# Kernel tuning notes

Measured on AMD Instinct MI355X. Metric: run time of the kernel, lower is better.

The kernel has to match this reference:

```python
import jax, jax.numpy as jnp
import numpy as np
from jax.ops import segment_sum, segment_max

DIM = 64
NUM_FEAT = 14
EDGE_FEAT = 4
OUT_DIM = 16
NUM_GRAPHS = 512
NEG_SLOPE = 0.01


def _leaky(v):
    return jnp.where(v >= 0, v, NEG_SLOPE * v)


def setup_inputs() -> dict:
    key = jax.random.key(0)
    ks = jax.random.split(key, 24)
    N, E = 20000, 40000
    s = 0.1
    inp = {
        "x": jax.random.normal(ks[0], (N, NUM_FEAT), jnp.float32),
        "edge_attr": jax.random.normal(ks[1], (E, EDGE_FEAT), jnp.float32),
        "edge_index": jax.random.randint(ks[2], (2, E), 0, N, jnp.int64) if jax.config.jax_enable_x64 else jax.random.randint(ks[2], (2, E), 0, N).astype(jnp.int32),
        "batch": jnp.sort(jax.random.randint(ks[3], (N,), 0, NUM_GRAPHS)).astype(jnp.int32),
        # lin0
        "lin0_w": s * jax.random.normal(ks[4], (DIM, NUM_FEAT), jnp.float32),
        "lin0_b": s * jax.random.normal(ks[5], (DIM,), jnp.float32),
        # edge network: Linear(4,dim) -> LeakyReLU -> Linear(dim, dim*dim)
        "net_w1": s * jax.random.normal(ks[6], (DIM, EDGE_FEAT), jnp.float32),
        "net_b1": s * jax.random.normal(ks[7], (DIM,), jnp.float32),
        "net_w2": s * jax.random.normal(ks[8], (DIM * DIM, DIM), jnp.float32),
        "net_b2": s * jax.random.normal(ks[9], (DIM * DIM,), jnp.float32),
        # NNConv root weight + bias
        "root_w": s * jax.random.normal(ks[10], (DIM, DIM), jnp.float32),
        "conv_b": s * jax.random.normal(ks[11], (DIM,), jnp.float32),
        # GRU (torch gate order: r, z, n)
        "gru_w_ih": s * jax.random.normal(ks[12], (3 * DIM, DIM), jnp.float32),
        "gru_w_hh": s * jax.random.normal(ks[13], (3 * DIM, DIM), jnp.float32),
        "gru_b_ih": s * jax.random.normal(ks[14], (3 * DIM,), jnp.float32),
        "gru_b_hh": s * jax.random.normal(ks[15], (3 * DIM,), jnp.float32),
        # Set2Set LSTM (input 2*dim, hidden dim; torch gate order: i, f, g, o)
        "lstm_w_ih": s * jax.random.normal(ks[16], (4 * DIM, 2 * DIM), jnp.float32),
        "lstm_w_hh": s * jax.random.normal(ks[17], (4 * DIM, DIM), jnp.float32),
        "lstm_b_ih": s * jax.random.normal(ks[18], (4 * DIM,), jnp.float32),
        "lstm_b_hh": s * jax.random.normal(ks[19], (4 * DIM,), jnp.float32),
        # lin_out
        "lout_w": s * jax.random.normal(ks[20], (OUT_DIM, 2 * DIM), jnp.float32),
        "lout_b": s * jax.random.normal(ks[21], (OUT_DIM,), jnp.float32),
    }
    return inp


def _forward(x, edge_attr, lin0_w, lin0_b, net_w1, net_b1, net_w2, net_b2,
             root_w, conv_b, gru_w_ih, gru_w_hh, gru_b_ih, gru_b_hh,
             lstm_w_ih, lstm_w_hh, lstm_b_ih, lstm_b_hh, lout_w, lout_b,
             edge_index, batch):
    N = x.shape[0]
    src, tgt = edge_index[0], edge_index[1]

    # per-edge dim x dim weight (shared across the 6 steps; edge_attr is static)
    ew = _leaky(edge_attr @ net_w1.T + net_b1) @ net_w2.T + net_b2  # [E, dim*dim]
    ew = ew.reshape(-1, DIM, DIM)  # [E, in, out]

    deg = segment_sum(jnp.ones_like(tgt, jnp.float32), tgt, num_segments=N)
    inv_deg = 1.0 / jnp.maximum(deg, 1.0)

    out = _leaky(x @ lin0_w.T + lin0_b)  # [N, dim]
    h = out
    for _ in range(6):
        msg = jnp.einsum('ed,edo->eo', out[src], ew)  # gather + per-edge matvec
        agg = segment_sum(msg, tgt, num_segments=N) * inv_deg[:, None]  # scatter-mean
        conv = agg + out @ root_w + conv_b
        m = _leaky(conv)
        # GRU cell (seq len 1)
        gi = m @ gru_w_ih.T + gru_b_ih
        gh = h @ gru_w_hh.T + gru_b_hh
        gi_r, gi_z, gi_n = jnp.split(gi, 3, axis=-1)
        gh_r, gh_z, gh_n = jnp.split(gh, 3, axis=-1)
        r = jax.nn.sigmoid(gi_r + gh_r)
        z = jax.nn.sigmoid(gi_z + gh_z)
        n = jnp.tanh(gi_n + r * gh_n)
        h = (1.0 - z) * n + z * h
        out = h

    # Set2Set, processing_steps=1
    B = NUM_GRAPHS
    q_star = jnp.zeros((B, 2 * DIM), x.dtype)
    h_l = jnp.zeros((B, DIM), x.dtype)
    c_l = jnp.zeros((B, DIM), x.dtype)
    gates = q_star @ lstm_w_ih.T + lstm_b_ih + h_l @ lstm_w_hh.T + lstm_b_hh
    gi_, gf_, gg_, go_ = jnp.split(gates, 4, axis=-1)
    i_g = jax.nn.sigmoid(gi_)
    f_g = jax.nn.sigmoid(gf_)
    g_g = jnp.tanh(gg_)
    o_g = jax.nn.sigmoid(go_)
    c = f_g * c_l + i_g * g_g
    q = o_g * jnp.tanh(c)  # [B, dim]

    e = jnp.sum(out * q[batch], axis=-1)  # [N]
    emax = segment_max(e, batch, num_segments=B)
    emax = jnp.where(jnp.isfinite(emax), emax, 0.0)
    ex = jnp.exp(e - emax[batch])
    denom = segment_sum(ex, batch, num_segments=B)
    a = ex / jnp.maximum(denom, 1e-16)[batch]
    r_read = segment_sum(a[:, None] * out, batch, num_segments=B)  # [B, dim]
    q_star = jnp.concatenate([q, r_read], axis=-1)  # [B, 2*dim]

    return q_star @ lout_w.T + lout_b  # [B, out_dim]


def reference(x, edge_attr, edge_index, batch, lin0_w, lin0_b, net_w1, net_b1,
              net_w2, net_b2, root_w, conv_b, gru_w_ih, gru_w_hh, gru_b_ih,
              gru_b_hh, lstm_w_ih, lstm_w_hh, lstm_b_ih, lstm_b_hh, lout_w, lout_b):
    return _forward(x, edge_attr, lin0_w, lin0_b, net_w1, net_b1, net_w2, net_b2,
                    root_w, conv_b, gru_w_ih, gru_w_hh, gru_b_ih, gru_b_hh,
                    lstm_w_ih, lstm_w_hh, lstm_b_ih, lstm_b_hh, lout_w, lout_b,
                    edge_index, batch)
```

## Files before the change

kernel.cpp:

```cpp
#include <hip/hip_runtime.h>
#include <math.h>

#define DIM 64
#define NFEAT 14
#define EFEAT 4
#define ODIM 16
#define NGRAPH 512
#define NEG 0.01f
#define EBLK 128
#define DSPLIT 4

typedef _Float16 f16;
typedef _Float16 f16x8 __attribute__((ext_vector_type(8)));
typedef float f32x4 __attribute__((ext_vector_type(4)));

#define MFMA(a,b,c) __builtin_amdgcn_mfma_f32_16x16x32_f16(a,b,c,0,0,0)

__device__ __forceinline__ float leaky(float v){ return v >= 0.f ? v : NEG*v; }
__device__ __forceinline__ float sigm(float v){ return 1.f/(1.f+expf(-v)); }

__global__ void k_pack(const float* __restrict__ src, f16* __restrict__ dst, int NC, int transB){
    int i = blockIdx.x*blockDim.x + threadIdx.x;
    if (i >= NC*64) return;
    int j = i & 7, l = (i >> 3) & 63, s = (i >> 9) & 1, CT = i >> 10;
    int k = ((l >> 4) << 3) + 32*s + j;
    int c = CT*16 + (l & 15);
    float v = transB ? src[(size_t)k*NC + c] : src[(size_t)c*64 + k];
    dst[i] = (f16)v;
}

__global__ void k_hid(const float* __restrict__ ea, const float* __restrict__ w1,
                      const float* __restrict__ b1, f16* __restrict__ hid16, int E){
    int i = blockIdx.x*blockDim.x + threadIdx.x;
    if (i >= E*DIM) return;
    int e = i >> 6, k = i & 63;
    const float* a = ea + (size_t)e*EFEAT;
    const float* w = w1 + k*EFEAT;
    float v = b1[k] + a[0]*w[0] + a[1]*w[1] + a[2]*w[2] + a[3]*w[3];
    hid16[i] = (f16)leaky(v);
}

__global__ void k_deg(const int* __restrict__ ei, float* __restrict__ deg, int E){
    int e = blockIdx.x*blockDim.x + threadIdx.x;
    if (e < E) atomicAdd(&deg[ei[E + e]], 1.0f);
}

__global__ void k_invdeg(float* __restrict__ deg, int N){
    int i = blockIdx.x*blockDim.x + threadIdx.x;
    if (i < N) deg[i] = 1.0f / fmaxf(deg[i], 1.0f);
}

__global__ void k_lin0(const float* __restrict__ x, const float* __restrict__ w,
                       const float* __restrict__ b, float* __restrict__ hf,
                       f16* __restrict__ out16, int N){
    int i = blockIdx.x*blockDim.x + threadIdx.x;
    if (i >= N*DIM) return;
    int n = i >> 6, o = i & 63;
    const float* xr = x + (size_t)n*NFEAT;
    const float* wr = w + o*NFEAT;
    float v = b[o];
#pragma unroll
    for (int f = 0; f < NFEAT; ++f) v += xr[f]*wr[f];
    v = leaky(v);
    hf[i] = v; out16[i] = (f16)v;
}

__global__ __launch_bounds__(256) void k_nbias(const f16x8* __restrict__ out16v,
                                               const f16x8* __restrict__ b2f,
                                               float* __restrict__ nb, int N){
    int n0 = blockIdx.x*64;
    int tid = threadIdx.x, w = tid >> 6, l = tid & 63, li = l & 15, lh = l >> 4;
    int ar = n0 + 16*w + li;
    f16x8 a0{}, a1{};
    if (ar < N){ a0 = out16v[(size_t)ar*8 + lh]; a1 = out16v[(size_t)ar*8 + lh + 4]; }
    f32x4 z = {0.f,0.f,0.f,0.f};
#pragma unroll
    for (int ct = 0; ct < 4; ++ct){
        f32x4 p = MFMA(a0, b2f[(ct*2+0)*64 + l], z);
        p = MFMA(a1, b2f[(ct*2+1)*64 + l], p);
#pragma unroll
        for (int reg = 0; reg < 4; ++reg){
            int n = n0 + 16*w + lh*4 + reg;
            if (n < N) nb[(size_t)n*64 + ct*16 + li] = p[reg];
        }
    }
}

__global__ __launch_bounds__(256) void k_fmsg(const float* __restrict__ hf,
                                              const f16x8* __restrict__ hid16v,
                                              const f16x8* __restrict__ wpf,
                                              const float* __restrict__ nb,
                                              const int* __restrict__ ei,
                                              float* __restrict__ agg, int E){
    __shared__ float Os[EBLK][20];
    __shared__ int ssrc[EBLK];
    __shared__ int stgt[EBLK];
    int tid = threadIdx.x;
    int e0 = blockIdx.x*EBLK;
    int dz = blockIdx.y;
    int d0 = dz*16;
    if (tid < EBLK){
        int e = e0 + tid;
        ssrc[tid] = (e < E) ? ei[e] : -1;
        stgt[tid] = (e < E) ? ei[E + e] : -1;
    }
    __syncthreads();
    for (int i = tid; i < EBLK*16; i += 256){
        int row = i >> 4, dl = i & 15;
        int s = ssrc[row];
        Os[row][dl] = (s >= 0) ? hf[(size_t)s*64 + d0 + dl] : 0.f;
    }

    int w = tid >> 6, l = tid & 63, li = l & 15, lh = l >> 4;
    f16x8 a[2][2];
#pragma unroll
    for (int rt = 0; rt < 2; ++rt){
        int e = e0 + w*32 + rt*16 + li;
        if (e < E){
            a[rt][0] = hid16v[(size_t)e*8 + lh];
            a[rt][1] = hid16v[(size_t)e*8 + lh + 4];
        } else { a[rt][0] = f16x8{}; a[rt][1] = f16x8{}; }
    }
    __syncthreads();

    float acc[2][4][4] = {};
    f32x4 z = {0.f,0.f,0.f,0.f};

#pragma unroll 2
    for (int dd = 0; dd < 16; ++dd){
        const f16x8* wrow = wpf + ((size_t)(d0 + dd))*512;
        f16x8 b[4][2];
#pragma unroll
        for (int ct = 0; ct < 4; ++ct){
            b[ct][0] = wrow[(ct*2+0)*64 + l];
            b[ct][1] = wrow[(ct*2+1)*64 + l];
        }
        float osv[2][4];
#pragma unroll
        for (int rt = 0; rt < 2; ++rt)
#pragma unroll
            for (int reg = 0; reg < 4; ++reg)
                osv[rt][reg] = Os[w*32 + rt*16 + lh*4 + reg][dd];
#pragma unroll
        for (int rt = 0; rt < 2; ++rt){
#pragma unroll
            for (int ct = 0; ct < 4; ++ct){
                f32x4 p = MFMA(a[rt][0], b[ct][0], z);
                p = MFMA(a[rt][1], b[ct][1], p);
#pragma unroll
                for (int reg = 0; reg < 4; ++reg)
                    acc[rt][ct][reg] += osv[rt][reg]*p[reg];
            }
        }
    }

#pragma unroll
    for (int rt = 0; rt < 2; ++rt){
#pragma unroll
        for (int reg = 0; reg < 4; ++reg){
            int row = w*32 + rt*16 + lh*4 + reg;
            int t = stgt[row];
            if (t < 0) continue;
            int s = ssrc[row];
#pragma unroll
            for (int ct = 0; ct < 4; ++ct){
                int col = ct*16 + li;
                float v = acc[rt][ct][reg];
                if (dz == 0) v += nb[(size_t)s*64 + col];
                atomicAdd(&agg[(size_t)t*64 + col], v);
            }
        }
    }
}

__global__ __launch_bounds__(256) void k_node(float* __restrict__ hf,
                                              f16* __restrict__ out16,
                                              const f16x8* __restrict__ out16v,
                                              float* __restrict__ agg,
                                              const float* __restrict__ invdeg,
                                              const float* __restrict__ convb,
                                              const f16x8* __restrict__ wrf,
                                              const f16x8* __restrict__ wihf,
                                              const f16x8* __restrict__ whhf,
                                              const float* __restrict__ bih,
                                              const float* __restrict__ bhh,
                                              const f16x8* __restrict__ b2f,
                                              float* __restrict__ nb, int N){
    __shared__ f16 Ms[64][72];
    int n0 = blockIdx.x*64;
    int tid = threadIdx.x, w = tid >> 6, l = tid & 63, li = l & 15, lh = l >> 4;
    f32x4 z = {0.f,0.f,0.f,0.f};

    int ar = n0 + 16*w + li;
    f16x8 a0{}, a1{};
    if (ar < N){ a0 = out16v[(size_t)ar*8 + lh]; a1 = out16v[(size_t)ar*8 + lh + 4]; }

    int nrow[4]; float invd[4];
#pragma unroll
    for (int reg = 0; reg < 4; ++reg){
        nrow[reg] = n0 + 16*w + lh*4 + reg;
        invd[reg] = (nrow[reg] < N) ? invdeg[nrow[reg]] : 0.f;
    }

#pragma unroll
    for (int ct = 0; ct < 4; ++ct){
        f32x4 p = MFMA(a0, wrf[(ct*2+0)*64 + l], z);
        p = MFMA(a1, wrf[(ct*2+1)*64 + l], p);
        int col = ct*16 + li;
        float cb = convb[col];
#pragma unroll
        for (int reg = 0; reg < 4; ++reg){
            int n = nrow[reg];
            float m = 0.f;
            if (n < N){
                size_t idx = (size_t)n*64 + col;
                m = leaky(p[reg] + agg[idx]*invd[reg] + cb);
                agg[idx] = 0.f;
            }
            Ms[16*w + lh*4 + reg][col] = (f16)m;
        }
    }
    __syncthreads();

    f16x8 am0 = *(const f16x8*)&Ms[16*w + li][lh*8];
    f16x8 am1 = *(const f16x8*)&Ms[16*w + li][lh*8 + 32];

#pragma unroll
    for (int ctq = 0; ctq < 4; ++ctq){
        int col = ctq*16 + li;
        f32x4 pir = MFMA(am0, wihf[((ctq+0)*2+0)*64 + l], z);
        pir = MFMA(am1, wihf[((ctq+0)*2+1)*64 + l], pir);
        f32x4 piz = MFMA(am0, wihf[((ctq+4)*2+0)*64 + l], z);
        piz = MFMA(am1, wihf[((ctq+4)*2+1)*64 + l], piz);
        f32x4 pin = MFMA(am0, wihf[((ctq+8)*2+0)*64 + l], z);
        pin = MFMA(am1, wihf[((ctq+8)*2+1)*64 + l], pin);
        f32x4 phr = MFMA(a0, whhf[((ctq+0)*2+0)*64 + l], z);
        phr = MFMA(a1, whhf[((ctq+0)*2+1)*64 + l], phr);
        f32x4 phz = MFMA(a0, whhf[((ctq+4)*2+0)*64 + l], z);
        phz = MFMA(a1, whhf[((ctq+4)*2+1)*64 + l], phz);
        f32x4 phn = MFMA(a0, whhf[((ctq+8)*2+0)*64 + l], z);
        phn = MFMA(a1, whhf[((ctq+8)*2+1)*64 + l], phn);
        float bir = bih[col], biz = bih[64+col], bin = bih[128+col];
        float bhr = bhh[col], bhz = bhh[64+col], bhn = bhh[128+col];
        __syncthreads();
#pragma unroll
        for (int reg = 0; reg < 4; ++reg){
            int n = nrow[reg];
            float hnew = 0.f;
            if (n < N){
                float hv = hf[(size_t)n*64 + col];
                float r  = sigm(pir[reg] + bir + phr[reg] + bhr);
                float zz = sigm(piz[reg] + biz + phz[reg] + bhz);
                float nn = tanhf(pin[reg] + bin + r*(phn[reg] + bhn));
                hnew = (1.f - zz)*nn + zz*hv;
                hf[(size_t)n*64 + col] = hnew;
                out16[(size_t)n*64 + col] = (f16)hnew;
            }
            Ms[16*w + lh*4 + reg][col] = (f16)hnew;
        }
    }
    __syncthreads();

    f16x8 an0 = *(const f16x8*)&Ms[16*w + li][lh*8];
    f16x8 an1 = *(const f16x8*)&Ms[16*w + li][lh*8 + 32];
#pragma unroll
    for (int ct = 0; ct < 4; ++ct){
        f32x4 p = MFMA(an0, b2f[(ct*2+0)*64 + l], z);
        p = MFMA(an1, b2f[(ct*2+1)*64 + l], p);
#pragma unroll
        for (int reg = 0; reg < 4; ++reg){
            int n = nrow[reg];
            if (n < N) nb[(size_t)n*64 + ct*16 + li] = p[reg];
        }
    }
}

__global__ void k_q(const float* __restrict__ bih, const float* __restrict__ bhh,
                    float* __restrict__ q){
    int j = threadIdx.x;
    if (j >= 64) return;
    float gi = bih[j]       + bhh[j];
    float gg = bih[128+j]   + bhh[128+j];
    float go = bih[192+j]   + bhh[192+j];
    float c = sigm(gi)*tanhf(gg);
    q[j] = sigm(go)*tanhf(c);
}

__device__ __forceinline__ unsigned fkey(float f){
    unsigned u = __float_as_uint(f);
    return (u >> 31) ? ~u : (u | 0x80000000u);
}

__global__ void k_edot(const float* __restrict__ out, const float* __restrict__ q,
                       const int* __restrict__ batch, float* __restrict__ ebuf,
                       unsigned* __restrict__ emaxk, int N){
    int gw = (blockIdx.x*blockDim.x + threadIdx.x) >> 6;
    int d = threadIdx.x & 63;
    if (gw >= N) return;
    float v = out[(size_t)gw*64 + d] * q[d];
#pragma unroll
    for (int s = 32; s; s >>= 1) v += __shfl_xor(v, s, 64);
    if (d == 0){
        ebuf[gw] = v;
        atomicMax(&emaxk[batch[gw]], fkey(v));
    }
}

__global__ void k_ex(float* __restrict__ ebuf, const unsigned* __restrict__ emaxk,
                     const int* __restrict__ batch, float* __restrict__ denom, int N){
    int n = blockIdx.x*blockDim.x + threadIdx.x;
    if (n >= N) return;
    int b = batch[n];
    unsigned k = emaxk[b];
    float em = (k == 0u) ? 0.f
             : ((k >> 31) ? __uint_as_float(k ^ 0x80000000u) : __uint_as_float(~k));
    float ex = expf(ebuf[n] - em);
    ebuf[n] = ex;
    atomicAdd(&denom[b], ex);
}

__global__ void k_rr(const float* __restrict__ out, const float* __restrict__ ebuf,
                     const float* __restrict__ denom, const int* __restrict__ batch,
                     float* __restrict__ rr, int N){
    int gw = (blockIdx.x*blockDim.x + threadIdx.x) >> 6;
    int o = threadIdx.x & 63;
    if (gw >= N) return;
    int b = batch[gw];
    float a = ebuf[gw] / fmaxf(denom[b], 1e-16f);
    atomicAdd(&rr[(size_t)b*64 + o], a * out[(size_t)gw*64 + o]);
}

__global__ void k_out(const float* __restrict__ q, const float* __restrict__ rr,
                      const float* __restrict__ lw, const float* __restrict__ lb,
                      float* __restrict__ dout){
    int i = blockIdx.x*blockDim.x + threadIdx.x;
    if (i >= NGRAPH*ODIM) return;
    int b = i / ODIM, j = i % ODIM;
    const float* w = lw + j*128;
    float acc = lb[j];
#pragma unroll 8
    for (int d = 0; d < 64; ++d) acc += w[d]*q[d];
    const float* rb = rr + (size_t)b*64;
#pragma unroll 8
    for (int d = 0; d < 64; ++d) acc += w[64+d]*rb[d];
    dout[i] = acc;
}

extern "C" void kernel_launch(void* const* d_in, const int* in_sizes, int n_in,
                              void* d_out, int out_size, void* d_ws, size_t ws_size,
                              hipStream_t stream){
    const float* x     = (const float*)d_in[0];
    const float* ea    = (const float*)d_in[1];
    const int*   ei    = (const int*)  d_in[2];
    const int*   batch = (const int*)  d_in[3];
    const float* lin0w = (const float*)d_in[4];
    const float* lin0b = (const float*)d_in[5];
    const float* w1    = (const float*)d_in[6];
    const float* b1    = (const float*)d_in[7];
    const float* w2    = (const float*)d_in[8];
    const float* b2    = (const float*)d_in[9];
    const float* rootw = (const float*)d_in[10];
    const float* convb = (const float*)d_in[11];
    const float* gwih  = (const float*)d_in[12];
    const float* gwhh  = (const float*)d_in[13];
    const float* gbih  = (const float*)d_in[14];
    const float* gbhh  = (const float*)d_in[15];
    const float* lsbih = (const float*)d_in[18];
    const float* lsbhh = (const float*)d_in[19];
    const float* loutw = (const float*)d_in[20];
    const float* loutb = (const float*)d_in[21];

    int N = in_sizes[0] / NFEAT;
    int E = in_sizes[1] / EFEAT;

    char* p = (char*)d_ws;
    size_t off = 0;
    auto carve = [&](size_t bytes) -> void* {
        void* r = p + off;
        off += (bytes + 255) & ~(size_t)255;
        return r;
    };
    f16*      hid16  = (f16*)     carve((size_t)E*64*2);
    float*    hf     = (float*)   carve((size_t)N*64*4);
    f16*      out16  = (f16*)     carve((size_t)N*64*2);
    float*    agg    = (float*)   carve((size_t)N*64*4);
    float*    nb     = (float*)   carve((size_t)N*64*4);
    float*    invdeg = (float*)   carve((size_t)N*4);
    float*    qv     = (float*)   carve(64*4);
    float*    ebuf   = (float*)   carve((size_t)N*4);
    unsigned* emaxk  = (unsigned*)carve(NGRAPH*4);
    float*    denom  = (float*)   carve(NGRAPH*4);
    float*    rr     = (float*)   carve((size_t)NGRAPH*64*4);
    f16*      wpf    = (f16*)     carve((size_t)4096*64*2);
    f16*      wrf    = (f16*)     carve(64*64*2);
    f16*      b2f    = (f16*)     carve(64*64*2);
    f16*      wihf   = (f16*)     carve(192*64*2);
    f16*      whhf   = (f16*)     carve(192*64*2);

    hipMemsetAsync(invdeg, 0, (size_t)N*4, stream);
    hipMemsetAsync(emaxk, 0, NGRAPH*4, stream);
    hipMemsetAsync(denom, 0, NGRAPH*4, stream);
    hipMemsetAsync(rr,    0, (size_t)NGRAPH*64*4, stream);
    hipMemsetAsync(agg,   0, (size_t)N*64*4, stream);

    k_pack<<<(4096*64 + 255)/256, 256, 0, stream>>>(w2,    wpf,  4096, 0);
    k_pack<<<(64*64   + 255)/256, 256, 0, stream>>>(rootw, wrf,  64,   1);
    k_pack<<<(64*64   + 255)/256, 256, 0, stream>>>(b2,    b2f,  64,   1);
    k_pack<<<(192*64  + 255)/256, 256, 0, stream>>>(gwih,  wihf, 192,  0);
    k_pack<<<(192*64  + 255)/256, 256, 0, stream>>>(gwhh,  whhf, 192,  0);

    k_hid<<<((size_t)E*64 + 255)/256, 256, 0, stream>>>(ea, w1, b1, hid16, E);
    k_deg<<<(E + 255)/256, 256, 0, stream>>>(ei, invdeg, E);
    k_invdeg<<<(N + 255)/256, 256, 0, stream>>>(invdeg, N);
    k_lin0<<<((size_t)N*64 + 255)/256, 256, 0, stream>>>(x, lin0w, lin0b, hf, out16, N);

    int eb  = (E + EBLK - 1)/EBLK;
    int nbk = (N + 63)/64;
    int node_grid = ((size_t)N*64 + 255)/256;

    k_nbias<<<nbk, 256, 0, stream>>>((const f16x8*)out16, (const f16x8*)b2f, nb, N);
    for (int it = 0; it < 6; ++it){
        k_fmsg<<<dim3(eb, DSPLIT), 256, 0, stream>>>(hf, (const f16x8*)hid16,
                                                     (const f16x8*)wpf, nb, ei, agg, E);
        k_node<<<nbk, 256, 0, stream>>>(hf, out16, (const f16x8*)out16, agg, invdeg,
                                        convb, (const f16x8*)wrf, (const f16x8*)wihf,
                                        (const f16x8*)whhf, gbih, gbhh,
                                        (const f16x8*)b2f, nb, N);
    }

    k_q<<<1, 64, 0, stream>>>(lsbih, lsbhh, qv);
    k_edot<<<node_grid, 256, 0, stream>>>(hf, qv, batch, ebuf, emaxk, N);
    k_ex<<<(N + 255)/256, 256, 0, stream>>>(ebuf, emaxk, batch, denom, N);
    k_rr<<<node_grid, 256, 0, stream>>>(hf, ebuf, denom, batch, rr, N);
    k_out<<<(NGRAPH*ODIM + 255)/256, 256, 0, stream>>>(qv, rr, loutw, loutb, (float*)d_out);
}
```

Baseline: 590.0 us.

## Stage edge-network weights in double-buffered LDS and drop DSPLIT grid split

Measured after the change: 555.0 us. 1.06x faster.

```diff
diff --git a/kernel.cpp b/kernel.cpp
--- a/kernel.cpp
+++ b/kernel.cpp
@@ -7,8 +7,7 @@
 #define ODIM 16
 #define NGRAPH 512
 #define NEG 0.01f
-#define EBLK 128
-#define DSPLIT 4
+#define EBLK 160
 
 typedef _Float16 f16;
 typedef _Float16 f16x8 __attribute__((ext_vector_type(8)));
@@ -86,31 +85,29 @@
     }
 }
 
-__global__ __launch_bounds__(256) void k_fmsg(const float* __restrict__ hf,
+__global__ __launch_bounds__(320) void k_fmsg(const float* __restrict__ hf,
                                               const f16x8* __restrict__ hid16v,
                                               const f16x8* __restrict__ wpf,
                                               const float* __restrict__ nb,
                                               const int* __restrict__ ei,
                                               float* __restrict__ agg, int E){
-    __shared__ float Os[EBLK][20];
+    __shared__ f16x8 Wch[2][2048];
+    __shared__ float OsT[64][164];
     __shared__ int ssrc[EBLK];
     __shared__ int stgt[EBLK];
     int tid = threadIdx.x;
     int e0 = blockIdx.x*EBLK;
-    int dz = blockIdx.y;
-    int d0 = dz*16;
     if (tid < EBLK){
         int e = e0 + tid;
         ssrc[tid] = (e < E) ? ei[e] : -1;
         stgt[tid] = (e < E) ? ei[E + e] : -1;
     }
     __syncthreads();
-    for (int i = tid; i < EBLK*16; i += 256){
-        int row = i >> 4, dl = i & 15;
-        int s = ssrc[row];
-        Os[row][dl] = (s >= 0) ? hf[(size_t)s*64 + d0 + dl] : 0.f;
-    }
-
+    for (int i = tid; i < EBLK*64; i += 320){
+        int r = i >> 6, d = i & 63;
+        int s = ssrc[r];
+        OsT[d][r] = (s >= 0) ? hf[(size_t)s*64 + d] : 0.f;
+    }
     int w = tid >> 6, l = tid & 63, li = l & 15, lh = l >> 4;
     f16x8 a[2][2];
 #pragma unroll
@@ -121,36 +118,62 @@
             a[rt][1] = hid16v[(size_t)e*8 + lh + 4];
         } else { a[rt][0] = f16x8{}; a[rt][1] = f16x8{}; }
     }
-    __syncthreads();
+    for (int i = tid; i < 2048; i += 320) Wch[0][i] = wpf[i];
 
     float acc[2][4][4] = {};
     f32x4 z = {0.f,0.f,0.f,0.f};
-
-#pragma unroll 2
-    for (int dd = 0; dd < 16; ++dd){
-        const f16x8* wrow = wpf + ((size_t)(d0 + dd))*512;
-        f16x8 b[4][2];
-#pragma unroll
-        for (int ct = 0; ct < 4; ++ct){
-            b[ct][0] = wrow[(ct*2+0)*64 + l];
-            b[ct][1] = wrow[(ct*2+1)*64 + l];
-        }
-        float osv[2][4];
-#pragma unroll
-        for (int rt = 0; rt < 2; ++rt)
-#pragma unroll
-            for (int reg = 0; reg < 4; ++reg)
-                osv[rt][reg] = Os[w*32 + rt*16 + lh*4 + reg][dd];
-#pragma unroll
-        for (int rt = 0; rt < 2; ++rt){
+    __syncthreads();
+
+    for (int c = 0; c < 16; ++c){
+        int cb = c & 1;
+        f16x8 p0{},p1{},p2{},p3{},p4{},p5{},p6{};
+        if (c < 15){
+            const f16x8* src = wpf + (size_t)(c+1)*2048;
+            p0 = src[tid];
+            p1 = src[tid + 320];
+            p2 = src[tid + 640];
+            p3 = src[tid + 960];
+            p4 = src[tid + 1280];
+            p5 = src[tid + 1600];
+            if (tid < 128) p6 = src[tid + 1920];
+        }
+#pragma unroll
+        for (int dd = 0; dd < 4; ++dd){
+            int d = c*4 + dd;
+            f16x8 b[4][2];
 #pragma unroll
             for (int ct = 0; ct < 4; ++ct){
-                f32x4 p = MFMA(a[rt][0], b[ct][0], z);
-                p = MFMA(a[rt][1], b[ct][1], p);
-#pragma unroll
-                for (int reg = 0; reg < 4; ++reg)
-                    acc[rt][ct][reg] += osv[rt][reg]*p[reg];
+                b[ct][0] = Wch[cb][(dd*8 + ct*2 + 0)*64 + l];
+                b[ct][1] = Wch[cb][(dd*8 + ct*2 + 1)*64 + l];
             }
+            float4 osv0 = *(const float4*)&OsT[d][w*32 + lh*4];
+            float4 osv1 = *(const float4*)&OsT[d][w*32 + 16 + lh*4];
+            float os0[4] = {osv0.x, osv0.y, osv0.z, osv0.w};
+            float os1[4] = {osv1.x, osv1.y, osv1.z, osv1.w};
+#pragma unroll
+            for (int ct = 0; ct < 4; ++ct){
+                f32x4 q0 = MFMA(a[0][0], b[ct][0], z);
+                q0 = MFMA(a[0][1], b[ct][1], q0);
+                f32x4 q1 = MFMA(a[1][0], b[ct][0], z);
+                q1 = MFMA(a[1][1], b[ct][1], q1);
+#pragma unroll
+                for (int reg = 0; reg < 4; ++reg){
+                    acc[0][ct][reg] += os0[reg]*q0[reg];
+                    acc[1][ct][reg] += os1[reg]*q1[reg];
+                }
+            }
+        }
+        if (c < 15){
+            __syncthreads();
+            int nbuf = cb ^ 1;
+            Wch[nbuf][tid]        = p0;
+            Wch[nbuf][tid + 320]  = p1;
+            Wch[nbuf][tid + 640]  = p2;
+            Wch[nbuf][tid + 960]  = p3;
+            Wch[nbuf][tid + 1280] = p4;
+            Wch[nbuf][tid + 1600] = p5;
+            if (tid < 128) Wch[nbuf][tid + 1920] = p6;
+            __syncthreads();
         }
     }
 
@@ -165,9 +188,7 @@
 #pragma unroll
             for (int ct = 0; ct < 4; ++ct){
                 int col = ct*16 + li;
-                float v = acc[rt][ct][reg];
-                if (dz == 0) v += nb[(size_t)s*64 + col];
-                atomicAdd(&agg[(size_t)t*64 + col], v);
+                atomicAdd(&agg[(size_t)t*64 + col], acc[rt][ct][reg] + nb[(size_t)s*64 + col]);
             }
         }
     }
@@ -420,8 +441,8 @@
 
     k_nbias<<<nbk, 256, 0, stream>>>((const f16x8*)out16, (const f16x8*)b2f, nb, N);
     for (int it = 0; it < 6; ++it){
-        k_fmsg<<<dim3(eb, DSPLIT), 256, 0, stream>>>(hf, (const f16x8*)hid16,
-                                                     (const f16x8*)wpf, nb, ei, agg, E);
+        k_fmsg<<<eb, 320, 0, stream>>>(hf, (const f16x8*)hid16, (const f16x8*)wpf,
+                                       nb, ei, agg, E);
         k_node<<<nbk, 256, 0, stream>>>(hf, out16, (const f16x8*)out16, agg, invdeg,
                                         convb, (const f16x8*)wrf, (const f16x8*)wihf,
                                         (const f16x8*)whhf, gbih, gbhh,
```

## Stage edge-network weights in LDS and fold source features into MFMA operands

Applied to the files above, without the earlier changes.

After: 589.4 us. Within noise of the previous version (-0.1%).

```diff
diff --git a/kernel.cpp b/kernel.cpp
--- a/kernel.cpp
+++ b/kernel.cpp
@@ -7,7 +7,7 @@
 #define ODIM 16
 #define NGRAPH 512
 #define NEG 0.01f
-#define EBLK 128
+#define EBLK 256
 #define DSPLIT 4
 
 typedef _Float16 f16;
@@ -86,79 +86,92 @@
     }
 }
 
-__global__ __launch_bounds__(256) void k_fmsg(const float* __restrict__ hf,
-                                              const f16x8* __restrict__ hid16v,
-                                              const f16x8* __restrict__ wpf,
-                                              const float* __restrict__ nb,
-                                              const int* __restrict__ ei,
-                                              float* __restrict__ agg, int E){
-    __shared__ float Os[EBLK][20];
+__global__ __launch_bounds__(256, 2) void k_fmsg(const float* __restrict__ hf,
+                                                 const f16x8* __restrict__ hid16v,
+                                                 const f16x8* __restrict__ wpf,
+                                                 const float* __restrict__ nb,
+                                                 const int* __restrict__ ei,
+                                                 float* __restrict__ agg, int E){
+    __shared__ f16x8 Wlds[2048];
+    __shared__ f16 OsT[EBLK][24];
     __shared__ int ssrc[EBLK];
     __shared__ int stgt[EBLK];
     int tid = threadIdx.x;
     int e0 = blockIdx.x*EBLK;
     int dz = blockIdx.y;
-    int d0 = dz*16;
-    if (tid < EBLK){
+    int dbase = dz*16;
+    {
         int e = e0 + tid;
         ssrc[tid] = (e < E) ? ei[e] : -1;
         stgt[tid] = (e < E) ? ei[E + e] : -1;
     }
     __syncthreads();
-    for (int i = tid; i < EBLK*16; i += 256){
-        int row = i >> 4, dl = i & 15;
-        int s = ssrc[row];
-        Os[row][dl] = (s >= 0) ? hf[(size_t)s*64 + d0 + dl] : 0.f;
+    {
+        int s = ssrc[tid];
+        float tmpf[16];
+#pragma unroll
+        for (int j = 0; j < 16; ++j) tmpf[j] = 0.f;
+        if (s >= 0){
+            const float4* hp = (const float4*)(hf + (size_t)s*64 + dbase);
+            *(float4*)&tmpf[0]  = hp[0];
+            *(float4*)&tmpf[4]  = hp[1];
+            *(float4*)&tmpf[8]  = hp[2];
+            *(float4*)&tmpf[12] = hp[3];
+        }
+        f16 tmph[16];
+#pragma unroll
+        for (int j = 0; j < 16; ++j) tmph[j] = (f16)tmpf[j];
+        *(f16x8*)&OsT[tid][0] = *(f16x8*)&tmph[0];
+        *(f16x8*)&OsT[tid][8] = *(f16x8*)&tmph[8];
     }
 
     int w = tid >> 6, l = tid & 63, li = l & 15, lh = l >> 4;
-    f16x8 a[2][2];
-#pragma unroll
-    for (int rt = 0; rt < 2; ++rt){
-        int e = e0 + w*32 + rt*16 + li;
+    f16x8 a[4][2];
+#pragma unroll
+    for (int rt = 0; rt < 4; ++rt){
+        int e = e0 + w*64 + rt*16 + li;
         if (e < E){
             a[rt][0] = hid16v[(size_t)e*8 + lh];
             a[rt][1] = hid16v[(size_t)e*8 + lh + 4];
         } else { a[rt][0] = f16x8{}; a[rt][1] = f16x8{}; }
     }
-    __syncthreads();
-
-    float acc[2][4][4] = {};
-    f32x4 z = {0.f,0.f,0.f,0.f};
-
-#pragma unroll 2
-    for (int dd = 0; dd < 16; ++dd){
-        const f16x8* wrow = wpf + ((size_t)(d0 + dd))*512;
-        f16x8 b[4][2];
-#pragma unroll
-        for (int ct = 0; ct < 4; ++ct){
-            b[ct][0] = wrow[(ct*2+0)*64 + l];
-            b[ct][1] = wrow[(ct*2+1)*64 + l];
-        }
-        float osv[2][4];
-#pragma unroll
-        for (int rt = 0; rt < 2; ++rt)
-#pragma unroll
-            for (int reg = 0; reg < 4; ++reg)
-                osv[rt][reg] = Os[w*32 + rt*16 + lh*4 + reg][dd];
-#pragma unroll
-        for (int rt = 0; rt < 2; ++rt){
+
+    f32x4 acc[4][4] = {};
+
+    for (int c = 0; c < 4; ++c){
+        __syncthreads();
+        const f16x8* src = wpf + (size_t)(dbase + c*4)*512;
+#pragma unroll
+        for (int i = 0; i < 8; ++i) Wlds[tid + i*256] = src[tid + i*256];
+        __syncthreads();
+#pragma unroll
+        for (int dd = 0; dd < 4; ++dd){
+            int dl = c*4 + dd;
+            f16x8 as[4][2];
+#pragma unroll
+            for (int rt = 0; rt < 4; ++rt){
+                f16 s = OsT[w*64 + rt*16 + li][dl];
+                as[rt][0] = a[rt][0]*s;
+                as[rt][1] = a[rt][1]*s;
+            }
 #pragma unroll
             for (int ct = 0; ct < 4; ++ct){
-                f32x4 p = MFMA(a[rt][0], b[ct][0], z);
-                p = MFMA(a[rt][1], b[ct][1], p);
-#pragma unroll
-                for (int reg = 0; reg < 4; ++reg)
-                    acc[rt][ct][reg] += osv[rt][reg]*p[reg];
+                f16x8 b0 = Wlds[(dd*8 + ct*2 + 0)*64 + l];
+                f16x8 b1 = Wlds[(dd*8 + ct*2 + 1)*64 + l];
+#pragma unroll
+                for (int rt = 0; rt < 4; ++rt){
+                    acc[rt][ct] = MFMA(as[rt][0], b0, acc[rt][ct]);
+                    acc[rt][ct] = MFMA(as[rt][1], b1, acc[rt][ct]);
+                }
             }
         }
     }
 
 #pragma unroll
-    for (int rt = 0; rt < 2; ++rt){
+    for (int rt = 0; rt < 4; ++rt){
 #pragma unroll
         for (int reg = 0; reg < 4; ++reg){
-            int row = w*32 + rt*16 + lh*4 + reg;
+            int row = w*64 + rt*16 + lh*4 + reg;
             int t = stgt[row];
             if (t < 0) continue;
             int s = ssrc[row];
@@ -383,25 +396,23 @@
     f16*      hid16  = (f16*)     carve((size_t)E*64*2);
     float*    hf     = (float*)   carve((size_t)N*64*4);
     f16*      out16  = (f16*)     carve((size_t)N*64*2);
-    float*    agg    = (float*)   carve((size_t)N*64*4);
     float*    nb     = (float*)   carve((size_t)N*64*4);
-    float*    invdeg = (float*)   carve((size_t)N*4);
     float*    qv     = (float*)   carve(64*4);
     float*    ebuf   = (float*)   carve((size_t)N*4);
-    unsigned* emaxk  = (unsigned*)carve(NGRAPH*4);
-    float*    denom  = (float*)   carve(NGRAPH*4);
-    float*    rr     = (float*)   carve((size_t)NGRAPH*64*4);
     f16*      wpf    = (f16*)     carve((size_t)4096*64*2);
     f16*      wrf    = (f16*)     carve(64*64*2);
     f16*      b2f    = (f16*)     carve(64*64*2);
     f16*      wihf   = (f16*)     carve(192*64*2);
     f16*      whhf   = (f16*)     carve(192*64*2);
-
-    hipMemsetAsync(invdeg, 0, (size_t)N*4, stream);
-    hipMemsetAsync(emaxk, 0, NGRAPH*4, stream);
-    hipMemsetAsync(denom, 0, NGRAPH*4, stream);
-    hipMemsetAsync(rr,    0, (size_t)NGRAPH*64*4, stream);
-    hipMemsetAsync(agg,   0, (size_t)N*64*4, stream);
+    size_t zero_beg = off;
+    float*    agg    = (float*)   carve((size_t)N*64*4);
+    float*    invdeg = (float*)   carve((size_t)N*4);
+    unsigned* emaxk  = (unsigned*)carve(NGRAPH*4);
+    float*    denom  = (float*)   carve(NGRAPH*4);
+    float*    rr     = (float*)   carve((size_t)NGRAPH*64*4);
+    size_t zero_end = off;
+
+    hipMemsetAsync(p + zero_beg, 0, zero_end - zero_beg, stream);
 
     k_pack<<<(4096*64 + 255)/256, 256, 0, stream>>>(w2,    wpf,  4096, 0);
     k_pack<<<(64*64   + 255)/256, 256, 0, stream>>>(rootw, wrf,  64,   1);
```
